# Performance work log

Measured on AMD Instinct MI355X. Metric: run time of the kernel, lower is better.

The kernel has to match this reference:

```python
import jax, jax.numpy as jnp
import numpy as np

D = 128
B = 512
N = 512
MAX_HOPS = 3


def _masked_softmax(v, mask, axis):
    m = jnp.max(v, axis=axis, keepdims=True)
    e = jnp.exp(v - m) * mask
    s = jnp.sum(e, axis=axis, keepdims=True) + 1e-5
    return e / s


def _l2_norm(x):
    # torch renorm(p=2, dim=0, maxnorm=1e-12).mul(1e12): rows with norm>maxnorm -> x/norm,
    # rows with norm<=maxnorm stay unchanged then *1e12
    maxnorm = 1e-12
    norm = jnp.sqrt(jnp.sum(x * x, axis=1, keepdims=True))
    safe = jnp.maximum(norm, maxnorm)
    return jnp.where(norm > maxnorm, x / safe, x * (1.0 / maxnorm))


def setup_inputs() -> dict:
    key = jax.random.key(0)
    ks = jax.random.split(key, 12)
    xavier = lambda k, shp: jax.random.uniform(k, shp, jnp.float32, -1.0, 1.0) * np.sqrt(6.0 / (shp[0] + shp[1]))
    return {
        "e1_embeded": jax.random.normal(ks[0], (B, D), jnp.float32),
        "rel_embeded": jax.random.normal(ks[1], (B, D), jnp.float32),
        "nei_embeded_key": jax.random.normal(ks[2], (B, N, D), jnp.float32),
        "nei_embeded_value": jax.random.normal(ks[3], (B, N, D), jnp.float32),
        "nei_mask": jax.random.randint(ks[4], (B, N), 0, 2, jnp.int32),
        "Wk": xavier(ks[5], (D, D)),
        "Wv": xavier(ks[6], (D, D)),
        "W_lin": xavier(ks[7], (D, D)),
        "b_lin": jnp.zeros((D,), jnp.float32),
        "W_att": xavier(ks[8], (3 * D, D)),
        "b_att": jnp.zeros((D,), jnp.float32),
        "dim": 2,
    }


def reference(e1_embeded, rel_embeded, nei_embeded_key, nei_embeded_value, nei_mask,
              Wk, Wv, W_lin, b_lin, W_att, b_att, dim):
    mask = nei_mask.astype(jnp.float32)  # [B,N]
    fk = jnp.einsum('bnd,de->bne', nei_embeded_key * mask[..., None], Wk)   # [B,N,D]
    fv = jnp.einsum('bnd,de->bne', nei_embeded_value * mask[..., None], Wv)  # [B,N,D]
    n = fk.shape[1]
    rel_b = jnp.broadcast_to(rel_embeded[:, None, :], fk.shape)
    u = e1_embeded
    for _ in range(MAX_HOPS):
        u_batch = jax.nn.leaky_relu(u @ W_lin + b_lin)                      # [B,D]
        ent_b = jnp.broadcast_to(u[:, None, :], fk.shape)
        m = jnp.concatenate([fk, ent_b, rel_b], axis=2)                      # [B,N,3D]
        att = jnp.sum(jax.nn.leaky_relu(jnp.einsum('bnk,kd->bnd', m, W_att) + b_att), axis=2)  # [B,N]
        p = _masked_softmax(att, mask, axis=1)
        o = jnp.sum(fv * p[..., None], axis=1)                               # [B,D]
        u = _l2_norm(u_batch + o)
    return u
```

## Files before the change

### kernel.cpp

```cpp
#include <hip/hip_runtime.h>

#define D 128
#define NN 512
#define BB 512

typedef __attribute__((ext_vector_type(8))) short short8;
typedef __attribute__((ext_vector_type(4))) float f32x4;

__device__ __forceinline__ unsigned int fbits(float f) {
  union { float f; unsigned int u; } v; v.f = f; return v.u;
}
__device__ __forceinline__ float ubits(unsigned int u) {
  union { unsigned int u; float f; } v; v.u = u; return v.f;
}
__device__ __forceinline__ unsigned short f2bf(float f) {
  unsigned int x = fbits(f);
  return (unsigned short)((x + 0x7fffu + ((x >> 16) & 1u)) >> 16);
}
__device__ __forceinline__ float h2f(unsigned short u) {
  _Float16 h; __builtin_memcpy(&h, &u, 2); return (float)h;
}
__device__ __forceinline__ unsigned short f2h(float f) {
  _Float16 h = (_Float16)f; unsigned short u; __builtin_memcpy(&u, &h, 2); return u;
}
__device__ __forceinline__ float lrelu(float x) { return x > 0.f ? x : 0.01f * x; }

__device__ __forceinline__ int fragidx(int k, int n) {
  return ((((n >> 4) * 4 + (k >> 5)) * 64 + ((k >> 3) & 3) * 16 + (n & 15)) << 3) + (k & 7);
}

__global__ __launch_bounds__(256) void prep_kernel(
    const float* __restrict__ Wk, const float* __restrict__ Watt,
    const float* __restrict__ batt, const float* __restrict__ rel,
    unsigned short* __restrict__ WhF, unsigned short* __restrict__ WlF,
    float* __restrict__ c3) {
  __shared__ float rowS[D];
  __shared__ float psum[2][D];
  const int blk = blockIdx.x;
  const int t = threadIdx.x;
  const float* src = (blk < D) ? (Wk + blk * D) : (rel + (blk - D) * D);
  const float* W   = (blk < D) ? Watt : (Watt + 2 * D * D);
  if (t < D) rowS[t] = src[t];
  __syncthreads();
  const int d = t & 127, half = t >> 7;
  const float* Wp = W + (half * 64) * D + d;
  float a = 0.f;
  #pragma unroll 8
  for (int k = 0; k < 64; ++k) a += rowS[half * 64 + k] * Wp[k * D];
  psum[half][d] = a;
  __syncthreads();
  if (t < D) {
    const float w = psum[0][t] + psum[1][t];
    if (blk < D) {
      const unsigned int ub = fbits(w);
      const int idx = fragidx(blk, t);
      WhF[idx] = (unsigned short)(ub >> 16);
      WlF[idx] = f2bf(w - ubits(ub & 0xFFFF0000u));
    } else {
      c3[(blk - D) * D + t] = w + batt[t];
    }
  }
}

__global__ __launch_bounds__(256) void gemm_g1_kernel(
    const float* __restrict__ key, const int* __restrict__ mask,
    const unsigned short* __restrict__ WhF, const unsigned short* __restrict__ WlF,
    unsigned short* __restrict__ g1h) {
  __shared__ __align__(16) unsigned short whlds[16384];
  __shared__ __align__(16) unsigned short wllds[16384];
  const int t = threadIdx.x;
  #pragma unroll
  for (int i = 0; i < 8; ++i) {
    const int unit = t + i * 256;
    *reinterpret_cast<uint4*>(&whlds[unit * 8]) = *reinterpret_cast<const uint4*>(WhF + unit * 8);
    *reinterpret_cast<uint4*>(&wllds[unit * 8]) = *reinterpret_cast<const uint4*>(WlF + unit * 8);
  }
  __syncthreads();
  const int wave = t >> 6, lane = t & 63;
  const int q = lane >> 4, l15 = lane & 15;
  const int ntiles = (BB * NN) / 64;
  for (int tile = blockIdx.x; tile < ntiles; tile += gridDim.x) {
    const long rowbase = (long)tile * 64 + wave * 16;
    const long r = rowbase + l15;
    const int mk = mask[r];
    short8 ah[4], al[4];
    #pragma unroll
    for (int kt = 0; kt < 4; ++kt) {
      const float* kp = key + r * D + kt * 32 + q * 8;
      float xs[8];
      *reinterpret_cast<float4*>(&xs[0]) = *reinterpret_cast<const float4*>(kp);
      *reinterpret_cast<float4*>(&xs[4]) = *reinterpret_cast<const float4*>(kp + 4);
      union { unsigned int u[4]; short8 v; } cvh, cvl;
      #pragma unroll
      for (int p2 = 0; p2 < 4; ++p2) {
        float a = xs[2 * p2], b = xs[2 * p2 + 1];
        if (!mk) { a = 0.f; b = 0.f; }
        const unsigned int ua = fbits(a), ub = fbits(b);
        cvh.u[p2] = (ua >> 16) | (ub & 0xFFFF0000u);
        const float ra = a - ubits(ua & 0xFFFF0000u);
        const float rb = b - ubits(ub & 0xFFFF0000u);
        cvl.u[p2] = (unsigned int)f2bf(ra) | ((unsigned int)f2bf(rb) << 16);
      }
      ah[kt] = cvh.v; al[kt] = cvl.v;
    }
    f32x4 acc[8];
    #pragma unroll
    for (int c = 0; c < 8; ++c) acc[c] = (f32x4){0.f, 0.f, 0.f, 0.f};
    #pragma unroll
    for (int kt = 0; kt < 4; ++kt) {
      #pragma unroll
      for (int c = 0; c < 8; ++c) {
        const short8 bh = *reinterpret_cast<const short8*>(&whlds[((c * 4 + kt) * 64 + lane) * 8]);
        const short8 bl = *reinterpret_cast<const short8*>(&wllds[((c * 4 + kt) * 64 + lane) * 8]);
        acc[c] = __builtin_amdgcn_mfma_f32_16x16x32_bf16(ah[kt], bh, acc[c], 0, 0, 0);
        acc[c] = __builtin_amdgcn_mfma_f32_16x16x32_bf16(al[kt], bh, acc[c], 0, 0, 0);
        acc[c] = __builtin_amdgcn_mfma_f32_16x16x32_bf16(ah[kt], bl, acc[c], 0, 0, 0);
      }
    }
    #pragma unroll
    for (int c = 0; c < 8; ++c) {
      #pragma unroll
      for (int reg = 0; reg < 4; ++reg) {
        const long row = rowbase + q * 4 + reg;
        g1h[row * D + c * 16 + l15] = f2h(acc[c][reg]);
      }
    }
  }
}

template <int USEVH>
__global__ __launch_bounds__(512, 4) void hops_kernel(
    const float* __restrict__ e1, const int* __restrict__ mask,
    const float* __restrict__ value, const unsigned short* __restrict__ g1h,
    unsigned short* __restrict__ vh,
    const float* __restrict__ Wlin, const float* __restrict__ blin,
    const float* __restrict__ Watt, const float* __restrict__ Wv,
    const float* __restrict__ c3, float* __restrict__ out) {
  __shared__ float uS[D], cS[D], ubS[D], opS[D];
  __shared__ float attS[NN];
  __shared__ float part[4][D];
  __shared__ float oscr[8][D];
  __shared__ float redA[8], redB[8];
  const int b = blockIdx.x;
  const int t = threadIdx.x;
  const int wv = t >> 6, lane = t & 63;
  const long base = (long)b * NN * D;
  const int* mb = mask + b * NN;
  if (t < D) uS[t] = e1[b * D + t];
  __syncthreads();
  for (int hop = 0; hop < 3; ++hop) {
    {
      const int d = t & 127, role = t >> 7;
      const float* W = (role < 2) ? (Watt + D * D) : Wlin;
      const int k0 = (role & 1) * 64;
      const float* Wp = W + k0 * D + d;
      float a = 0.f;
      #pragma unroll 8
      for (int k = 0; k < 64; ++k) a += uS[k0 + k] * Wp[k * D];
      part[role][d] = a;
    }
    __syncthreads();
    if (t < D) cS[t] = part[0][t] + part[1][t] + c3[b * D + t];
    else if (t < 2 * D) { const int d = t - D; ubS[d] = lrelu(part[2][d] + part[3][d] + blin[d]); }
    __syncthreads();
    {
      const int grp = t >> 4, l = t & 15, d0 = l * 8;
      float creg[8];
      #pragma unroll
      for (int j = 0; j < 8; ++j) creg[j] = cS[d0 + j];
      #pragma unroll 4
      for (int i = 0; i < 16; ++i) {
        const int n = i * 32 + grp;
        const uint4 raw = *reinterpret_cast<const uint4*>(g1h + base + (long)n * D + d0);
        const unsigned short* e = reinterpret_cast<const unsigned short*>(&raw);
        float s = 0.f;
        #pragma unroll
        for (int j = 0; j < 8; ++j) s += lrelu(h2f(e[j]) + creg[j]);
        #pragma unroll
        for (int off = 8; off > 0; off >>= 1) s += __shfl_xor(s, off, 16);
        if (l == 0) attS[n] = s;
      }
    }
    __syncthreads();
    {
      const float av = attS[t];
      float m = av;
      #pragma unroll
      for (int off = 32; off > 0; off >>= 1) m = fmaxf(m, __shfl_xor(m, off, 64));
      if (lane == 0) redA[wv] = m;
      __syncthreads();
      m = redA[0];
      #pragma unroll
      for (int w2 = 1; w2 < 8; ++w2) m = fmaxf(m, redA[w2]);
      const float e0 = __expf(av - m) * (mb[t] ? 1.f : 0.f);
      float ss = e0;
      #pragma unroll
      for (int off = 32; off > 0; off >>= 1) ss += __shfl_xor(ss, off, 64);
      if (lane == 0) redB[wv] = ss;
      __syncthreads();
      float s = 1e-5f;
      #pragma unroll
      for (int w2 = 0; w2 < 8; ++w2) s += redB[w2];
      attS[t] = e0 / s;
    }
    __syncthreads();
    {
      const int grp = t >> 4, l = t & 15, d0 = l * 8;
      float acc8[8];
      #pragma unroll
      for (int j = 0; j < 8; ++j) acc8[j] = 0.f;
      if (USEVH && hop == 0) {
        #pragma unroll 2
        for (int i = 0; i < 16; ++i) {
          const int n = i * 32 + grp;
          const float p = attS[n];
          float vv[8];
          *reinterpret_cast<float4*>(&vv[0]) = *reinterpret_cast<const float4*>(value + base + (long)n * D + d0);
          *reinterpret_cast<float4*>(&vv[4]) = *reinterpret_cast<const float4*>(value + base + (long)n * D + d0 + 4);
          unsigned short hv[8];
          #pragma unroll
          for (int j = 0; j < 8; ++j) { hv[j] = f2h(vv[j]); acc8[j] += p * vv[j]; }
          *reinterpret_cast<uint4*>(vh + base + (long)n * D + d0) = *reinterpret_cast<const uint4*>(hv);
        }
      } else if (USEVH) {
        #pragma unroll 4
        for (int i = 0; i < 16; ++i) {
          const int n = i * 32 + grp;
          const float p = attS[n];
          const uint4 raw = *reinterpret_cast<const uint4*>(vh + base + (long)n * D + d0);
          const unsigned short* e = reinterpret_cast<const unsigned short*>(&raw);
          #pragma unroll
          for (int j = 0; j < 8; ++j) acc8[j] += p * h2f(e[j]);
        }
      } else {
        #pragma unroll 2
        for (int i = 0; i < 16; ++i) {
          const int n = i * 32 + grp;
          const float p = attS[n];
          float vv[8];
          *reinterpret_cast<float4*>(&vv[0]) = *reinterpret_cast<const float4*>(value + base + (long)n * D + d0);
          *reinterpret_cast<float4*>(&vv[4]) = *reinterpret_cast<const float4*>(value + base + (long)n * D + d0 + 4);
          #pragma unroll
          for (int j = 0; j < 8; ++j) acc8[j] += p * vv[j];
        }
      }
      #pragma unroll
      for (int j = 0; j < 8; ++j) {
        acc8[j] += __shfl_xor(acc8[j], 16, 64);
        acc8[j] += __shfl_xor(acc8[j], 32, 64);
      }
      if (lane < 16) {
        #pragma unroll
        for (int j = 0; j < 8; ++j) oscr[wv][lane * 8 + j] = acc8[j];
      }
    }
    __syncthreads();
    if (t < D) {
      float s = 0.f;
      #pragma unroll
      for (int w2 = 0; w2 < 8; ++w2) s += oscr[w2][t];
      opS[t] = s;
    }
    __syncthreads();
    {
      const int d = t & 127, role = t >> 7;
      const int k0 = role * 32;
      const float* Wp = Wv + k0 * D + d;
      float a = 0.f;
      #pragma unroll 8
      for (int k = 0; k < 32; ++k) a += opS[k0 + k] * Wp[k * D];
      part[role][d] = a;
    }
    __syncthreads();
    {
      float un = 0.f, sq = 0.f;
      if (t < D) {
        un = ubS[t] + part[0][t] + part[1][t] + part[2][t] + part[3][t];
        sq = un * un;
      }
      #pragma unroll
      for (int off = 32; off > 0; off >>= 1) sq += __shfl_xor(sq, off, 64);
      if (lane == 0) redA[wv] = sq;
      __syncthreads();
      float ns = 0.f;
      #pragma unroll
      for (int w2 = 0; w2 < 8; ++w2) ns += redA[w2];
      const float norm = sqrtf(ns);
      const float inv = (norm > 1e-12f) ? (1.f / norm) : 1e12f;
      if (t < D) uS[t] = un * inv;
    }
    __syncthreads();
  }
  if (t < D) out[b * D + t] = uS[t];
}

extern "C" void kernel_launch(void* const* d_in, const int* in_sizes, int n_in,
                              void* d_out, int out_size, void* d_ws, size_t ws_size,
                              hipStream_t stream) {
  const float* e1   = (const float*)d_in[0];
  const float* rel  = (const float*)d_in[1];
  const float* key  = (const float*)d_in[2];
  const float* val  = (const float*)d_in[3];
  const int*   mask = (const int*)d_in[4];
  const float* Wk   = (const float*)d_in[5];
  const float* Wv   = (const float*)d_in[6];
  const float* Wlin = (const float*)d_in[7];
  const float* blin = (const float*)d_in[8];
  const float* Watt = (const float*)d_in[9];
  const float* batt = (const float*)d_in[10];
  float* out = (float*)d_out;

  char* ws = (char*)d_ws;
  unsigned short* WhF = (unsigned short*)ws;
  unsigned short* WlF = (unsigned short*)(ws + 32 * 1024);
  float*          c3  = (float*)(ws + 64 * 1024);
  unsigned short* g1h = (unsigned short*)(ws + 512 * 1024);
  const size_t g1bytes = (size_t)BB * NN * D * sizeof(unsigned short);
  unsigned short* vh  = (unsigned short*)(ws + 512 * 1024 + g1bytes);

  const size_t need_vh = 512 * 1024 + 2 * g1bytes;
  const bool usevh = (ws_size >= need_vh);

  prep_kernel<<<D + BB, 256, 0, stream>>>(Wk, Watt, batt, rel, WhF, WlF, c3);
  gemm_g1_kernel<<<1024, 256, 0, stream>>>(key, mask, WhF, WlF, g1h);
  if (usevh) {
    hops_kernel<1><<<BB, 512, 0, stream>>>(e1, mask, val, g1h, vh, Wlin, blin, Watt, Wv, c3, out);
  } else {
    hops_kernel<0><<<BB, 512, 0, stream>>>(e1, mask, val, g1h, vh, Wlin, blin, Watt, Wv, c3, out);
  }
}
```

Baseline: 393.5 us.

## Keep fp16 value cache in registers across hops instead of global workspace

On the first hop each thread converts its slice of the value tensor to fp16 and keeps it in a 16-entry uint4 register array. Later hops read those registers instead of writing and re-reading an fp16 copy in global workspace. This removes that extra global traffic and the template dispatch on workspace size. The attention-score loop now batches four g1 loads before computing, and the g1 GEMM grid is halved. The register array adds heavy register pressure under launch bounds of 4 blocks of 512 threads, so spilling is a risk, and the grid change depends on how the hidden GEMM kernel indexes its work.

```diff
diff --git a/kernel.cpp b/kernel.cpp
--- a/kernel.cpp
+++ b/kernel.cpp
@@ -128,11 +128,9 @@
   }
 }
 
-template <int USEVH>
 __global__ __launch_bounds__(512, 4) void hops_kernel(
     const float* __restrict__ e1, const int* __restrict__ mask,
     const float* __restrict__ value, const unsigned short* __restrict__ g1h,
-    unsigned short* __restrict__ vh,
     const float* __restrict__ Wlin, const float* __restrict__ blin,
     const float* __restrict__ Watt, const float* __restrict__ Wv,
     const float* __restrict__ c3, float* __restrict__ out) {
@@ -144,8 +142,10 @@
   const int b = blockIdx.x;
   const int t = threadIdx.x;
   const int wv = t >> 6, lane = t & 63;
+  const int grp = t >> 4, l = t & 15, d0 = (t & 15) * 8;
   const long base = (long)b * NN * D;
   const int* mb = mask + b * NN;
+  uint4 vr[16];
   if (t < D) uS[t] = e1[b * D + t];
   __syncthreads();
   for (int hop = 0; hop < 3; ++hop) {
@@ -164,21 +164,28 @@
     else if (t < 2 * D) { const int d = t - D; ubS[d] = lrelu(part[2][d] + part[3][d] + blin[d]); }
     __syncthreads();
     {
-      const int grp = t >> 4, l = t & 15, d0 = l * 8;
       float creg[8];
       #pragma unroll
       for (int j = 0; j < 8; ++j) creg[j] = cS[d0 + j];
-      #pragma unroll 4
-      for (int i = 0; i < 16; ++i) {
-        const int n = i * 32 + grp;
-        const uint4 raw = *reinterpret_cast<const uint4*>(g1h + base + (long)n * D + d0);
-        const unsigned short* e = reinterpret_cast<const unsigned short*>(&raw);
-        float s = 0.f;
-        #pragma unroll
-        for (int j = 0; j < 8; ++j) s += lrelu(h2f(e[j]) + creg[j]);
-        #pragma unroll
-        for (int off = 8; off > 0; off >>= 1) s += __shfl_xor(s, off, 16);
-        if (l == 0) attS[n] = s;
+      #pragma unroll
+      for (int ii = 0; ii < 4; ++ii) {
+        uint4 g[4];
+        #pragma unroll
+        for (int j2 = 0; j2 < 4; ++j2) {
+          const int n = (ii * 4 + j2) * 32 + grp;
+          g[j2] = *reinterpret_cast<const uint4*>(g1h + base + (long)n * D + d0);
+        }
+        #pragma unroll
+        for (int j2 = 0; j2 < 4; ++j2) {
+          const int n = (ii * 4 + j2) * 32 + grp;
+          const unsigned short* e = reinterpret_cast<const unsigned short*>(&g[j2]);
+          float s = 0.f;
+          #pragma unroll
+          for (int j = 0; j < 8; ++j) s += lrelu(h2f(e[j]) + creg[j]);
+          #pragma unroll
+          for (int off = 8; off > 0; off >>= 1) s += __shfl_xor(s, off, 16);
+          if (l == 0) attS[n] = s;
+        }
       }
     }
     __syncthreads();
@@ -205,43 +212,49 @@
     }
     __syncthreads();
     {
-      const int grp = t >> 4, l = t & 15, d0 = l * 8;
       float acc8[8];
       #pragma unroll
       for (int j = 0; j < 8; ++j) acc8[j] = 0.f;
-      if (USEVH && hop == 0) {
-        #pragma unroll 2
-        for (int i = 0; i < 16; ++i) {
-          const int n = i * 32 + grp;
-          const float p = attS[n];
-          float vv[8];
-          *reinterpret_cast<float4*>(&vv[0]) = *reinterpret_cast<const float4*>(value + base + (long)n * D + d0);
-          *reinterpret_cast<float4*>(&vv[4]) = *reinterpret_cast<const float4*>(value + base + (long)n * D + d0 + 4);
-          unsigned short hv[8];
+      if (hop == 0) {
+        #pragma unroll
+        for (int ii = 0; ii < 8; ++ii) {
+          float4 va[2], vb[2];
           #pragma unroll
-          for (int j = 0; j < 8; ++j) { hv[j] = f2h(vv[j]); acc8[j] += p * vv[j]; }
-          *reinterpret_cast<uint4*>(vh + base + (long)n * D + d0) = *reinterpret_cast<const uint4*>(hv);
-        }
-      } else if (USEVH) {
-        #pragma unroll 4
-        for (int i = 0; i < 16; ++i) {
-          const int n = i * 32 + grp;
-          const float p = attS[n];
-          const uint4 raw = *reinterpret_cast<const uint4*>(vh + base + (long)n * D + d0);
-          const unsigned short* e = reinterpret_cast<const unsigned short*>(&raw);
+          for (int j2 = 0; j2 < 2; ++j2) {
+            const int n = (ii * 2 + j2) * 32 + grp;
+            const float* vp = value + base + (long)n * D + d0;
+            va[j2] = *reinterpret_cast<const float4*>(vp);
+            vb[j2] = *reinterpret_cast<const float4*>(vp + 4);
+          }
           #pragma unroll
-          for (int j = 0; j < 8; ++j) acc8[j] += p * h2f(e[j]);
+          for (int j2 = 0; j2 < 2; ++j2) {
+            const int i = ii * 2 + j2;
+            const float p = attS[i * 32 + grp];
+            acc8[0] += p * va[j2].x; acc8[1] += p * va[j2].y;
+            acc8[2] += p * va[j2].z; acc8[3] += p * va[j2].w;
+            acc8[4] += p * vb[j2].x; acc8[5] += p * vb[j2].y;
+            acc8[6] += p * vb[j2].z; acc8[7] += p * vb[j2].w;
+            uint4 q;
+            q.x = (unsigned)f2h(va[j2].x) | ((unsigned)f2h(va[j2].y) << 16);
+            q.y = (unsigned)f2h(va[j2].z) | ((unsigned)f2h(va[j2].w) << 16);
+            q.z = (unsigned)f2h(vb[j2].x) | ((unsigned)f2h(vb[j2].y) << 16);
+            q.w = (unsigned)f2h(vb[j2].z) | ((unsigned)f2h(vb[j2].w) << 16);
+            vr[i] = q;
+          }
         }
       } else {
-        #pragma unroll 2
+        #pragma unroll
         for (int i = 0; i < 16; ++i) {
-          const int n = i * 32 + grp;
-          const float p = attS[n];
-          float vv[8];
-          *reinterpret_cast<float4*>(&vv[0]) = *reinterpret_cast<const float4*>(value + base + (long)n * D + d0);
-          *reinterpret_cast<float4*>(&vv[4]) = *reinterpret_cast<const float4*>(value + base + (long)n * D + d0 + 4);
-          #pragma unroll
-          for (int j = 0; j < 8; ++j) acc8[j] += p * vv[j];
+          const float p = attS[i * 32 + grp];
+          const uint4 q = vr[i];
+          acc8[0] += p * h2f((unsigned short)(q.x & 0xffffu));
+          acc8[1] += p * h2f((unsigned short)(q.x >> 16));
+          acc8[2] += p * h2f((unsigned short)(q.y & 0xffffu));
+          acc8[3] += p * h2f((unsigned short)(q.y >> 16));
+          acc8[4] += p * h2f((unsigned short)(q.z & 0xffffu));
+          acc8[5] += p * h2f((unsigned short)(q.z >> 16));
+          acc8[6] += p * h2f((unsigned short)(q.w & 0xffffu));
+          acc8[7] += p * h2f((unsigned short)(q.w >> 16));
         }
       }
       #pragma unroll
@@ -315,17 +328,8 @@
   unsigned short* WlF = (unsigned short*)(ws + 32 * 1024);
   float*          c3  = (float*)(ws + 64 * 1024);
   unsigned short* g1h = (unsigned short*)(ws + 512 * 1024);
-  const size_t g1bytes = (size_t)BB * NN * D * sizeof(unsigned short);
-  unsigned short* vh  = (unsigned short*)(ws + 512 * 1024 + g1bytes);
-
-  const size_t need_vh = 512 * 1024 + 2 * g1bytes;
-  const bool usevh = (ws_size >= need_vh);
 
   prep_kernel<<<D + BB, 256, 0, stream>>>(Wk, Watt, batt, rel, WhF, WlF, c3);
-  gemm_g1_kernel<<<1024, 256, 0, stream>>>(key, mask, WhF, WlF, g1h);
-  if (usevh) {
-    hops_kernel<1><<<BB, 512, 0, stream>>>(e1, mask, val, g1h, vh, Wlin, blin, Watt, Wv, c3, out);
-  } else {
-    hops_kernel<0><<<BB, 512, 0, stream>>>(e1, mask, val, g1h, vh, Wlin, blin, Watt, Wv, c3, out);
-  }
-}
+  gemm_g1_kernel<<<512, 256, 0, stream>>>(key, mask, WhF, WlF, g1h);
+  hops_kernel<<<BB, 512, 0, stream>>>(e1, mask, val, g1h, Wlin, blin, Watt, Wv, c3, out);
+}
```

New measurement: 594.6 us. +51.1%, slower.
